# Kernel optimization log

Hardware: AMD Instinct MI355X
Metric: run time of the kernel (lower is better)

Reference implementation:

```python
import jax, jax.numpy as jnp
import numpy as np

NUM_EXPERTS = 8
TOP_K = 2
ENTROPY_WEIGHT = 0.1
MAX_USAGE_RATIO = 0.3


def setup_inputs() -> dict:
    key = jax.random.key(0)
    k0, k1, k2 = jax.random.split(key, 3)
    B, S, D, H, E = 4, 4096, 1024, 1024, NUM_EXPERTS
    x = jax.random.normal(k0, (B, S, D), jnp.float32)
    gate_w = jax.random.normal(k1, (D, E), jnp.float32) * (1.0 / np.sqrt(D))
    gate_b = jnp.zeros((E,), jnp.float32)
    expert_w = jax.random.normal(k2, (E, D, H), jnp.float32) * (1.0 / np.sqrt(D))
    expert_b = jnp.zeros((E, H), jnp.float32)
    return {"x": x, "gate_w": gate_w, "gate_b": gate_b,
            "expert_w": expert_w, "expert_b": expert_b}


def reference(x, gate_w, gate_b, expert_w, expert_b):
    # x: [B, S, D]; dropout omitted (eval mode / deterministic reference)
    B, S, D = x.shape
    E = gate_w.shape[1]
    H = expert_w.shape[2]
    N = B * S
    xf = x.reshape(N, D)

    gate_logits = xf @ gate_w + gate_b            # [N, E]
    gate_probs = jax.nn.softmax(gate_logits, axis=-1)
    entropy = -jnp.sum(gate_probs * jnp.log(gate_probs + 1e-10), axis=-1).mean()
    entropy_loss = ENTROPY_WEIGHT * entropy

    topk_probs, topk_idx = jax.lax.top_k(gate_probs, TOP_K)   # [N, K]
    onehot = jax.nn.one_hot(topk_idx, E, dtype=xf.dtype)       # [N, K, E]
    combine = jnp.einsum('nk,nke->ne', topk_probs, onehot)     # [N, E] gating weight per expert

    # Weighted combine of per-expert Linear outputs; loop over small fixed E.
    out = jnp.zeros((N, H), xf.dtype)
    for e in range(E):
        out = out + combine[:, e:e + 1] * (xf @ expert_w[e] + expert_b[e])

    counts = jnp.sum(onehot, axis=(0, 1))                      # [E] tokens routed per expert
    usage_ratios = counts / N
    overuse_penalty = jnp.sum(jax.nn.relu(usage_ratios - MAX_USAGE_RATIO))

    return out.reshape(B, S, H), entropy_loss + overuse_penalty
```

## Files before the change

### kernel.cpp

```cpp
#include <hip/hip_runtime.h>
#include <hip/hip_bf16.h>

typedef __bf16 bf16x8 __attribute__((ext_vector_type(8)));
typedef __bf16 bf16x4 __attribute__((ext_vector_type(4)));
typedef float  f32x4  __attribute__((ext_vector_type(4)));

#define NTOK 16384
#define DDIM 1024
#define HDIM 1024

#define XB_OFF   0u
#define WT_OFF   33554432u
#define IDXP_OFF 50331648u
#define PPP_OFF  50397184u
#define TPID_OFF 50528256u
#define TPP_OFF  50593792u
#define CNTB_OFF 50724864u
#define ENTB_OFF 50790400u
#define TOT_OFF  50794496u

typedef __attribute__((address_space(1))) void gvoid_t;
typedef __attribute__((address_space(3))) void lvoid_t;

__device__ __forceinline__ void cp16(void* lds, const void* g) {
  __builtin_amdgcn_global_load_lds((gvoid_t*)g, (lvoid_t*)lds, 16, 0, 0);
}

__global__ __launch_bounds__(256) void prep_kernel(
    const float* __restrict__ ew, __bf16* __restrict__ wT,
    const float* __restrict__ x, const float* __restrict__ gw,
    const float* __restrict__ gb, __bf16* __restrict__ xb,
    int* __restrict__ tt_pid, float2* __restrict__ tt_pp,
    unsigned char* __restrict__ cnt_blk, float* __restrict__ ent_blk) {
  __shared__ __align__(16) char smem[33040];
  const int tid = threadIdx.x;

  if (blockIdx.x < 2048) {
    typedef float (*TileT)[69];
    TileT tile = (TileT)smem;
    const int b  = blockIdx.x;
    const int e  = b >> 8;
    const int d0 = ((b >> 4) & 15) * 64;
    const int h0 = (b & 15) * 64;
    const float* base = ew + ((size_t)e * DDIM + d0) * HDIM + h0;
#pragma unroll
    for (int it = 0; it < 4; ++it) {
      int dl = it * 16 + (tid >> 4);
      int hl = (tid & 15) * 4;
      float4 v = *(const float4*)(base + (size_t)dl * HDIM + hl);
      tile[dl][hl]     = v.x;
      tile[dl][hl + 1] = v.y;
      tile[dl][hl + 2] = v.z;
      tile[dl][hl + 3] = v.w;
    }
    __syncthreads();
    __bf16* obase = wT + ((size_t)e * HDIM + h0) * DDIM + d0;
#pragma unroll
    for (int it = 0; it < 2; ++it) {
      int hl = it * 32 + (tid >> 3);
      int dl = (tid & 7) * 8;
      bf16x8 bv;
#pragma unroll
      for (int i = 0; i < 8; ++i) bv[i] = (__bf16)tile[dl + i][hl];
      *(bf16x8*)(obase + (size_t)hl * DDIM + dl) = bv;
    }
    return;
  }

  float* gwT  = (float*)smem;
  int*   lcnt = (int*)(smem + 32768);
  float* went = (float*)(smem + 33024);
  const int bid = blockIdx.x - 2048;
  const int wv = tid >> 6, lane = tid & 63;
  for (int i = tid; i < 64; i += 256) lcnt[i] = 0;
#pragma unroll
  for (int i = 0; i < 32; ++i) {
    int lin = i * 256 + tid;
    gwT[(lin & 7) * 1024 + (lin >> 3)] = gw[lin];
  }
  __syncthreads();
  float4 gr[4][8];
#pragma unroll
  for (int j = 0; j < 4; ++j)
#pragma unroll
    for (int e = 0; e < 8; ++e)
      gr[j][e] = *(const float4*)&gwT[e * 1024 + j * 256 + lane * 4];
  float gbr[8];
#pragma unroll
  for (int e = 0; e < 8; ++e) gbr[e] = gb[e];

  float entacc = 0.f;
  for (int t = 0; t < 4; ++t) {
    const int n = bid * 16 + wv * 4 + t;
    float acc[8] = {0.f, 0.f, 0.f, 0.f, 0.f, 0.f, 0.f, 0.f};
#pragma unroll
    for (int j = 0; j < 4; ++j) {
      float4 v = *(const float4*)(x + (size_t)n * DDIM + j * 256 + lane * 4);
      bf16x4 bv;
      bv[0] = (__bf16)v.x; bv[1] = (__bf16)v.y;
      bv[2] = (__bf16)v.z; bv[3] = (__bf16)v.w;
      *(bf16x4*)(xb + (size_t)n * DDIM + j * 256 + lane * 4) = bv;
#pragma unroll
      for (int e = 0; e < 8; ++e) {
        float4 g = gr[j][e];
        acc[e] += v.x * g.x + v.y * g.y + v.z * g.z + v.w * g.w;
      }
    }
#pragma unroll
    for (int e = 0; e < 8; ++e) {
      float s = acc[e];
#pragma unroll
      for (int off = 1; off < 64; off <<= 1) s += __shfl_xor(s, off);
      acc[e] = s;
    }
    float p[8], lg[8];
    float mx = -1e30f;
#pragma unroll
    for (int e = 0; e < 8; ++e) { p[e] = acc[e] + gbr[e]; mx = fmaxf(mx, p[e]); }
    float s = 0.f;
#pragma unroll
    for (int e = 0; e < 8; ++e) { lg[e] = p[e] - mx; p[e] = expf(lg[e]); s += p[e]; }
    float inv = 1.0f / s;
    float dot = 0.f;
#pragma unroll
    for (int e = 0; e < 8; ++e) { p[e] *= inv; dot += p[e] * lg[e]; }
    entacc += logf(s) - dot;
    int e1 = 0; float p1 = p[0];
#pragma unroll
    for (int e = 1; e < 8; ++e) if (p[e] > p1) { p1 = p[e]; e1 = e; }
    int e2 = (e1 == 0) ? 1 : 0; float p2 = p[e2];
#pragma unroll
    for (int e = 0; e < 8; ++e) if (e != e1 && p[e] > p2) { p2 = p[e]; e2 = e; }
    int   elo = (e1 < e2) ? e1 : e2;
    int   ehi = (e1 < e2) ? e2 : e1;
    float plo = (e1 < e2) ? p1 : p2;
    float phi = (e1 < e2) ? p2 : p1;
    int pid = elo * 8 + ehi;
    if (lane == 0) {
      tt_pid[n] = pid;
      tt_pp[n]  = make_float2(plo, phi);
      atomicAdd(&lcnt[pid], 1);
    }
  }
  if (lane == 0) went[wv] = entacc;
  __syncthreads();
  if (tid < 64) cnt_blk[bid * 64 + tid] = (unsigned char)lcnt[tid];
  if (tid == 0) ent_blk[bid] = went[0] + went[1] + went[2] + went[3];
}

__global__ __launch_bounds__(256) void scatter_kernel(
    const int* __restrict__ tt_pid, const float2* __restrict__ tt_pp,
    const unsigned char* __restrict__ cnt_blk, const float* __restrict__ ent_blk,
    int* __restrict__ idx_p, float2* __restrict__ pp_p,
    int* __restrict__ tot_g, float* __restrict__ loss_out) {
  __shared__ int part_tot[4][64], part_off[4][64];
  __shared__ int tot_l[64], off_l[64], base_l[64], lcnt[64];
  __shared__ float esum[4];
  const int t = threadIdx.x, b = blockIdx.x;
  const int p = t & 63, q = t >> 6;
  const int bcut = b * 16;

  int s_tot = 0, s_off = 0;
  for (int i = 0; i < 256; ++i) {
    int bb = q * 256 + i;
    int c = cnt_blk[bb * 64 + p];
    s_tot += c;
    s_off += (bb < bcut) ? c : 0;
  }
  part_tot[q][p] = s_tot;
  part_off[q][p] = s_off;
  if (t < 64) lcnt[t] = 0;
  __syncthreads();
  if (t < 64) {
    tot_l[t] = part_tot[0][t] + part_tot[1][t] + part_tot[2][t] + part_tot[3][t];
    off_l[t] = part_off[0][t] + part_off[1][t] + part_off[2][t] + part_off[3][t];
  }
  __syncthreads();
  if (t < 64) {
    int base = 0;
    for (int i = 0; i < t; ++i) base += tot_l[i];
    base_l[t] = base;
  }
  const int n   = b * 256 + t;
  const int pid = tt_pid[n];
  const float2 pp = tt_pp[n];
  __syncthreads();
  int lofs = atomicAdd(&lcnt[pid], 1);
  int dst = base_l[pid] + off_l[pid] + lofs;
  idx_p[dst] = n;
  pp_p[dst]  = pp;

  if (b == 0) {
    if (t < 64) tot_g[t] = tot_l[t];
    float e = ent_blk[t] + ent_blk[t + 256] + ent_blk[t + 512] + ent_blk[t + 768];
#pragma unroll
    for (int off = 1; off < 64; off <<= 1) e += __shfl_xor(e, off);
    if ((t & 63) == 0) esum[t >> 6] = e;
    __syncthreads();
    if (t == 0) {
      float ent = esum[0] + esum[1] + esum[2] + esum[3];
      int ecnt[8] = {0, 0, 0, 0, 0, 0, 0, 0};
      for (int pd = 0; pd < 64; ++pd) {
        int c = tot_l[pd];
        ecnt[pd >> 3] += c;
        ecnt[pd & 7]  += c;
      }
      float pen = 0.f;
      for (int e8 = 0; e8 < 8; ++e8) {
        float r = (float)ecnt[e8] / (float)NTOK - 0.3f;
        if (r > 0.f) pen += r;
      }
      loss_out[0] = 0.1f * (ent / (float)NTOK) + pen;
    }
  }
}

__global__ __launch_bounds__(256) void moe_gemm(
    const __bf16* __restrict__ xb, const __bf16* __restrict__ wT,
    const float* __restrict__ eb, const int* __restrict__ idx_p,
    const float2* __restrict__ pp_p, const int* __restrict__ tot_g,
    float* __restrict__ out) {
  const int gy = blockIdx.y, gx = blockIdx.x;

  __shared__ __bf16 Ash[128 * 64];
  __shared__ __bf16 BloS[128 * 64];
  __shared__ __bf16 BhiS[128 * 64];
  __shared__ int    tok_s[128];
  __shared__ float2 pp_s[128];
  __shared__ int    tot_s[64];
  __shared__ int    hdr[4];

  const int tid = threadIdx.x, w = tid >> 6, lane = tid & 63;
  if (tid < 64) tot_s[tid] = tot_g[tid];
  __syncthreads();
  if (tid == 0) {
    int bacc = 0, ti = 0, fpid = -1, frow = 0, fcnt = 0, fbase = 0;
    for (int pd = 0; pd < 64; ++pd) {
      int c = tot_s[pd];
      if (c > 0) {
        int ntl = (c + 127) >> 7;
        if (gy >= ti && gy < ti + ntl) {
          fpid = pd; frow = (gy - ti) * 128; fcnt = c; fbase = bacc;
        }
        ti += ntl;
        bacc += c;
      }
    }
    hdr[0] = fpid; hdr[1] = frow; hdr[2] = fcnt; hdr[3] = fbase;
  }
  __syncthreads();
  const int pid = hdr[0];
  if (pid < 0) return;
  const int row0 = hdr[1], cntp = hdr[2], gbase = hdr[3];
  const int elo = pid >> 3, ehi = pid & 7;

  if (tid < 128) {
    int s = row0 + tid;
    int g = gbase + ((s < cntp) ? s : (cntp - 1));
    tok_s[tid] = idx_p[g];
    pp_s[tid]  = pp_p[g];
  }
  __syncthreads();

  f32x4 accL[4][4], accH[4][4];
  const f32x4 zero = {0.f, 0.f, 0.f, 0.f};
#pragma unroll
  for (int mi = 0; mi < 4; ++mi)
#pragma unroll
    for (int ni = 0; ni < 4; ++ni) { accL[mi][ni] = zero; accH[mi][ni] = zero; }

  const int wm = (w >> 1) * 64, wn = (w & 1) * 64;
  const int tq = lane >> 4, tr = lane & 15, tr7 = tr & 7;
  const int rsub = lane >> 3;
  const int csw = ((lane & 7) ^ rsub) * 8;

  const __bf16* wlo = wT + (size_t)elo * HDIM * DDIM + (size_t)(gx * 128) * DDIM;
  const __bf16* whi = wT + (size_t)ehi * HDIM * DDIM + (size_t)(gx * 128) * DDIM;
  const __bf16* aptr[4];
  const __bf16* lptr[4];
  const __bf16* hptr[4];
#pragma unroll
  for (int it = 0; it < 4; ++it) {
    int r = it * 32 + w * 8 + rsub;
    aptr[it] = xb + (size_t)tok_s[r] * DDIM + csw;
    lptr[it] = wlo + (size_t)r * DDIM + csw;
    hptr[it] = whi + (size_t)r * DDIM + csw;
  }

  for (int kk = 0; kk < 16; ++kk) {
#pragma unroll
    for (int it = 0; it < 4; ++it) {
      const int rb = it * 32 + w * 8;
      cp16((char*)Ash  + rb * 128, aptr[it]); aptr[it] += 64;
      cp16((char*)BloS + rb * 128, lptr[it]); lptr[it] += 64;
      cp16((char*)BhiS + rb * 128, hptr[it]); hptr[it] += 64;
    }
    __syncthreads();
#pragma unroll
    for (int h = 0; h < 2; ++h) {
      const int co = (h << 2) | tq;
      bf16x8 a[4], bl[4], bh[4];
#pragma unroll
      for (int mi = 0; mi < 4; ++mi)
        a[mi] = *(const bf16x8*)((const char*)Ash + (wm + mi * 16 + tr) * 128 +
                                 ((co ^ tr7) << 4));
#pragma unroll
      for (int ni = 0; ni < 4; ++ni) {
        bl[ni] = *(const bf16x8*)((const char*)BloS + (wn + ni * 16 + tr) * 128 +
                                  ((co ^ tr7) << 4));
        bh[ni] = *(const bf16x8*)((const char*)BhiS + (wn + ni * 16 + tr) * 128 +
                                  ((co ^ tr7) << 4));
      }
#pragma unroll
      for (int mi = 0; mi < 4; ++mi)
#pragma unroll
        for (int ni = 0; ni < 4; ++ni) {
          accL[mi][ni] = __builtin_amdgcn_mfma_f32_16x16x32_bf16(a[mi], bl[ni], accL[mi][ni], 0, 0, 0);
          accH[mi][ni] = __builtin_amdgcn_mfma_f32_16x16x32_bf16(a[mi], bh[ni], accH[mi][ni], 0, 0, 0);
        }
    }
    __syncthreads();
  }

  float blov[4], bhiv[4];
#pragma unroll
  for (int ni = 0; ni < 4; ++ni) {
    int col = gx * 128 + wn + ni * 16 + tr;
    blov[ni] = eb[elo * HDIM + col];
    bhiv[ni] = eb[ehi * HDIM + col];
  }
#pragma unroll
  for (int mi = 0; mi < 4; ++mi)
#pragma unroll
    for (int r = 0; r < 4; ++r) {
      int lr = wm + mi * 16 + tq * 4 + r;
      if (row0 + lr < cntp) {
        int    tok = tok_s[lr];
        float2 pp  = pp_s[lr];
        float* orow = out + (size_t)tok * HDIM + gx * 128 + wn + tr;
#pragma unroll
        for (int ni = 0; ni < 4; ++ni)
          orow[ni * 16] = pp.x * (accL[mi][ni][r] + blov[ni]) +
                          pp.y * (accH[mi][ni][r] + bhiv[ni]);
      }
    }
}

extern "C" void kernel_launch(void* const* d_in, const int* in_sizes, int n_in,
                              void* d_out, int out_size, void* d_ws, size_t ws_size,
                              hipStream_t stream) {
  const float* x  = (const float*)d_in[0];
  const float* gw = (const float*)d_in[1];
  const float* gb = (const float*)d_in[2];
  const float* ew = (const float*)d_in[3];
  const float* eb = (const float*)d_in[4];
  float* out = (float*)d_out;
  char*  ws  = (char*)d_ws;

  __bf16* xb     = (__bf16*)(ws + XB_OFF);
  __bf16* wT     = (__bf16*)(ws + WT_OFF);
  int*    idx_p  = (int*)(ws + IDXP_OFF);
  float2* pp_p   = (float2*)(ws + PPP_OFF);
  int*    tt_pid = (int*)(ws + TPID_OFF);
  float2* tt_pp  = (float2*)(ws + TPP_OFF);
  unsigned char* cnt_blk = (unsigned char*)(ws + CNTB_OFF);
  float*  ent_blk = (float*)(ws + ENTB_OFF);
  int*    tot_g   = (int*)(ws + TOT_OFF);

  prep_kernel<<<dim3(3072), 256, 0, stream>>>(ew, wT, x, gw, gb, xb,
                                              tt_pid, tt_pp, cnt_blk, ent_blk);
  scatter_kernel<<<dim3(64), 256, 0, stream>>>(tt_pid, tt_pp, cnt_blk, ent_blk,
                                               idx_p, pp_p, tot_g,
                                               out + (size_t)NTOK * HDIM);
  moe_gemm<<<dim3(8, 160), 256, 0, stream>>>(xb, wT, eb, idx_p, pp_p, tot_g,
                                             out);
}
```

Measured before the change: 331.3 us.

## Double-buffer K=32 LDS tiles in MoE GEMM and compute tile header via wave scan

Splits the K loop into 32 steps of width 32 and uses two LDS buffers, so the async global-to-LDS copies for the next step are issued before the MFMAs on the current step. This removes one barrier per iteration and overlaps load latency with compute. The serial single-thread tile-assignment loop is replaced by a wave-wide prefix scan with ballot, which drops two barriers at kernel start. Each step now does less MFMA work per barrier, and the LDS row swizzle changes to match the narrower 64-byte rows.

```diff
diff --git a/kernel.cpp b/kernel.cpp
--- a/kernel.cpp
+++ b/kernel.cpp
@@ -221,38 +221,34 @@
     const float2* __restrict__ pp_p, const int* __restrict__ tot_g,
     float* __restrict__ out) {
   const int gy = blockIdx.y, gx = blockIdx.x;
-
-  __shared__ __bf16 Ash[128 * 64];
-  __shared__ __bf16 BloS[128 * 64];
-  __shared__ __bf16 BhiS[128 * 64];
+  const int tid = threadIdx.x, w = tid >> 6, lane = tid & 63;
+
+  int c_pd = tot_g[lane];
+  int ntl  = (c_pd + 127) >> 7;
+  int cinc = c_pd, tinc = ntl;
+#pragma unroll
+  for (int off = 1; off < 64; off <<= 1) {
+    int vc = __shfl_up(cinc, off);
+    int vt = __shfl_up(tinc, off);
+    if (lane >= off) { cinc += vc; tinc += vt; }
+  }
+  const int cexc = cinc - c_pd;
+  const int texc = tinc - ntl;
+  bool own = (c_pd > 0) && (gy >= texc) && (gy < texc + ntl);
+  unsigned long long mask = __ballot(own);
+  if (mask == 0ull) return;
+  const int src  = (int)__builtin_ctzll(mask);
+  const int pid  = src;
+  const int cntp = __shfl(c_pd, src);
+  const int gbase = __shfl(cexc, src);
+  const int row0  = (gy - __shfl(texc, src)) * 128;
+  const int elo = pid >> 3, ehi = pid & 7;
+
+  __shared__ __bf16 Abuf[2][128 * 32];
+  __shared__ __bf16 Lbuf[2][128 * 32];
+  __shared__ __bf16 Hbuf[2][128 * 32];
   __shared__ int    tok_s[128];
   __shared__ float2 pp_s[128];
-  __shared__ int    tot_s[64];
-  __shared__ int    hdr[4];
-
-  const int tid = threadIdx.x, w = tid >> 6, lane = tid & 63;
-  if (tid < 64) tot_s[tid] = tot_g[tid];
-  __syncthreads();
-  if (tid == 0) {
-    int bacc = 0, ti = 0, fpid = -1, frow = 0, fcnt = 0, fbase = 0;
-    for (int pd = 0; pd < 64; ++pd) {
-      int c = tot_s[pd];
-      if (c > 0) {
-        int ntl = (c + 127) >> 7;
-        if (gy >= ti && gy < ti + ntl) {
-          fpid = pd; frow = (gy - ti) * 128; fcnt = c; fbase = bacc;
-        }
-        ti += ntl;
-        bacc += c;
-      }
-    }
-    hdr[0] = fpid; hdr[1] = frow; hdr[2] = fcnt; hdr[3] = fbase;
-  }
-  __syncthreads();
-  const int pid = hdr[0];
-  if (pid < 0) return;
-  const int row0 = hdr[1], cntp = hdr[2], gbase = hdr[3];
-  const int elo = pid >> 3, ehi = pid & 7;
 
   if (tid < 128) {
     int s = row0 + tid;
@@ -270,56 +266,62 @@
     for (int ni = 0; ni < 4; ++ni) { accL[mi][ni] = zero; accH[mi][ni] = zero; }
 
   const int wm = (w >> 1) * 64, wn = (w & 1) * 64;
-  const int tq = lane >> 4, tr = lane & 15, tr7 = tr & 7;
-  const int rsub = lane >> 3;
-  const int csw = ((lane & 7) ^ rsub) * 8;
+  const int tq = lane >> 4, tr = lane & 15;
+  const int rloc = lane >> 2;
+  const int cg   = lane & 3;
+  const int scol = (cg ^ (rloc & 3)) * 8;
 
   const __bf16* wlo = wT + (size_t)elo * HDIM * DDIM + (size_t)(gx * 128) * DDIM;
   const __bf16* whi = wT + (size_t)ehi * HDIM * DDIM + (size_t)(gx * 128) * DDIM;
-  const __bf16* aptr[4];
-  const __bf16* lptr[4];
-  const __bf16* hptr[4];
-#pragma unroll
-  for (int it = 0; it < 4; ++it) {
-    int r = it * 32 + w * 8 + rsub;
-    aptr[it] = xb + (size_t)tok_s[r] * DDIM + csw;
-    lptr[it] = wlo + (size_t)r * DDIM + csw;
-    hptr[it] = whi + (size_t)r * DDIM + csw;
-  }
-
-  for (int kk = 0; kk < 16; ++kk) {
-#pragma unroll
-    for (int it = 0; it < 4; ++it) {
-      const int rb = it * 32 + w * 8;
-      cp16((char*)Ash  + rb * 128, aptr[it]); aptr[it] += 64;
-      cp16((char*)BloS + rb * 128, lptr[it]); lptr[it] += 64;
-      cp16((char*)BhiS + rb * 128, hptr[it]); hptr[it] += 64;
-    }
-    __syncthreads();
-#pragma unroll
-    for (int h = 0; h < 2; ++h) {
-      const int co = (h << 2) | tq;
-      bf16x8 a[4], bl[4], bh[4];
-#pragma unroll
-      for (int mi = 0; mi < 4; ++mi)
-        a[mi] = *(const bf16x8*)((const char*)Ash + (wm + mi * 16 + tr) * 128 +
-                                 ((co ^ tr7) << 4));
+  const __bf16* aptr[2];
+  const __bf16* lptr[2];
+  const __bf16* hptr[2];
+  int dofs[2];
+#pragma unroll
+  for (int i = 0; i < 2; ++i) {
+    int r = (i * 4 + w) * 16 + rloc;
+    aptr[i] = xb + (size_t)tok_s[r] * DDIM + scol;
+    lptr[i] = wlo + (size_t)r * DDIM + scol;
+    hptr[i] = whi + (size_t)r * DDIM + scol;
+    dofs[i] = (i * 4 + w) * 1024;
+  }
+
+#pragma unroll
+  for (int i = 0; i < 2; ++i) {
+    cp16((char*)Abuf[0] + dofs[i], aptr[i]); aptr[i] += 32;
+    cp16((char*)Lbuf[0] + dofs[i], lptr[i]); lptr[i] += 32;
+    cp16((char*)Hbuf[0] + dofs[i], hptr[i]); hptr[i] += 32;
+  }
+  __syncthreads();
+
+  const int chq = (tq ^ (tr & 3)) << 4;
+  int bsel = 0;
+  for (int kk = 0; kk < 32; ++kk) {
+    if (kk < 31) {
+#pragma unroll
+      for (int i = 0; i < 2; ++i) {
+        cp16((char*)Abuf[bsel ^ 1] + dofs[i], aptr[i]); aptr[i] += 32;
+        cp16((char*)Lbuf[bsel ^ 1] + dofs[i], lptr[i]); lptr[i] += 32;
+        cp16((char*)Hbuf[bsel ^ 1] + dofs[i], hptr[i]); hptr[i] += 32;
+      }
+    }
+    bf16x8 a[4], bl[4], bh[4];
+#pragma unroll
+    for (int mi = 0; mi < 4; ++mi)
+      a[mi] = *(const bf16x8*)((const char*)Abuf[bsel] + (wm + mi * 16 + tr) * 64 + chq);
+#pragma unroll
+    for (int ni = 0; ni < 4; ++ni) {
+      bl[ni] = *(const bf16x8*)((const char*)Lbuf[bsel] + (wn + ni * 16 + tr) * 64 + chq);
+      bh[ni] = *(const bf16x8*)((const char*)Hbuf[bsel] + (wn + ni * 16 + tr) * 64 + chq);
+    }
+#pragma unroll
+    for (int mi = 0; mi < 4; ++mi)
 #pragma unroll
       for (int ni = 0; ni < 4; ++ni) {
-        bl[ni] = *(const bf16x8*)((const char*)BloS + (wn + ni * 16 + tr) * 128 +
-                                  ((co ^ tr7) << 4));
-        bh[ni] = *(const bf16x8*)((const char*)BhiS + (wn + ni * 16 + tr) * 128 +
-                                  ((co ^ tr7) << 4));
-      }
-#pragma unroll
-      for (int mi = 0; mi < 4; ++mi)
-#pragma unroll
-        for (int ni = 0; ni < 4; ++ni) {
-          accL[mi][ni] = __builtin_amdgcn_mfma_f32_16x16x32_bf16(a[mi], bl[ni], accL[mi][ni], 0, 0, 0);
-          accH[mi][ni] = __builtin_amdgcn_mfma_f32_16x16x32_bf16(a[mi], bh[ni], accH[mi][ni], 0, 0, 0);
-        }
-    }
-    __syncthreads();
+        accL[mi][ni] = __builtin_amdgcn_mfma_f32_16x16x32_bf16(a[mi], bl[ni], accL[mi][ni], 0, 0, 0);
+        accH[mi][ni] = __builtin_amdgcn_mfma_f32_16x16x32_bf16(a[mi], bh[ni], accH[mi][ni], 0, 0, 0);
+      }
+    if (kk < 31) { __syncthreads(); bsel ^= 1; }
   }
 
   float blov[4], bhiv[4];
```

Measured after the change: 310.6 us. -6.2%, faster.
